# Kernel optimization log

Measured on AMD Instinct MI355X. Metric: run time of the kernel, lower is better.

## Reference

```python
import jax, jax.numpy as jnp
import numpy as np

EMBED_DIM = 1024
NUM_HEADS = 16
HEAD_DIM = EMBED_DIM // NUM_HEADS
THRESHOLD = 0.001
B, S = 8, 1024


def setup_inputs() -> dict:
    key = jax.random.key(0)
    ks = jax.random.split(key, 7)
    sc = 1.0 / np.sqrt(EMBED_DIM)
    return {
        "x": jax.random.normal(ks[0], (B, S, EMBED_DIM), dtype=jnp.float32),
        "Wq": jax.random.normal(ks[1], (NUM_HEADS, EMBED_DIM, HEAD_DIM), dtype=jnp.float32) * sc,
        "bq": jax.random.normal(ks[2], (NUM_HEADS, HEAD_DIM), dtype=jnp.float32) * 0.01,
        "Wk": jax.random.normal(ks[3], (NUM_HEADS, EMBED_DIM, HEAD_DIM), dtype=jnp.float32) * sc,
        "bk": jax.random.normal(ks[4], (NUM_HEADS, HEAD_DIM), dtype=jnp.float32) * 0.01,
        "Wv": jax.random.normal(ks[5], (NUM_HEADS, EMBED_DIM, HEAD_DIM), dtype=jnp.float32) * sc,
        "bv": jax.random.normal(ks[6], (NUM_HEADS, HEAD_DIM), dtype=jnp.float32) * 0.01,
    }


def thresholded_softmax(scores, threshold):
    # softmax over last dim, zero entries below threshold, renormalize
    s = jax.nn.softmax(scores, axis=-1)
    s = jnp.where(s < threshold, 0.0, s)
    return s / (jnp.sum(s, axis=-1, keepdims=True) + 1e-12)


def reference(x, Wq, bq, Wk, bk, Wv, bv):
    # x: [B,S,D]; Wq/Wk/Wv: [H,D,e]; biases: [H,e]
    scale = jnp.asarray(EMBED_DIM ** 0.5, x.dtype)  # note: scales by sqrt(embed_dim), not head_dim
    Q = jnp.einsum("bsd,hde->hbse", x, Wq) + bq[:, None, None, :]
    K = jnp.einsum("bsd,hde->hbse", x, Wk) + bk[:, None, None, :]
    V = jnp.einsum("bsd,hde->hbse", x, Wv) + bv[:, None, None, :]
    scores = jnp.einsum("hbse,hbte->hbst", Q, K) / scale  # [H,B,S,S]
    att = thresholded_softmax(scores, THRESHOLD)
    latent = jnp.einsum("hbst,hbte->hbse", att, V)  # [H,B,S,e]
    # concat heads along last dim in head order -> [B,S,H*e]
    residual = jnp.transpose(latent, (1, 2, 0, 3)).reshape(x.shape[0], x.shape[1], -1)
    x_res = x + residual  # dropout p=0.0 -> identity
    return (x_res, att)
```

## Files before the change

### kernel.cpp

```cpp
#include <hip/hip_runtime.h>
#include <hip/hip_bf16.h>
#include <cstdint>
#include <cstddef>

#define B_ 8
#define S_ 1024
#define H_ 16
#define E_ 64
#define D_ 1024

typedef unsigned short u16;
typedef short s16x8 __attribute__((ext_vector_type(8)));
typedef float f32x4 __attribute__((ext_vector_type(4)));

__device__ __forceinline__ u16 f2b(float f) {
  union { float f; unsigned u; } v; v.f = f;
  unsigned u = v.u;
  return (u16)((u + 0x7FFFu + ((u >> 16) & 1u)) >> 16);
}

__device__ __forceinline__ void gload16(const void* g, void* lds) {
  __builtin_amdgcn_global_load_lds(
      (const __attribute__((address_space(1))) void*)g,
      (__attribute__((address_space(3))) void*)lds, 16, 0, 0);
}

#define BARL() do {                                          \
  asm volatile("s_waitcnt lgkmcnt(0)" ::: "memory");         \
  __builtin_amdgcn_sched_barrier(0);                         \
  __builtin_amdgcn_s_barrier();                              \
  __builtin_amdgcn_sched_barrier(0);                         \
  asm volatile("" ::: "memory");                             \
} while (0)

__global__ void k_prep(const float* __restrict__ x, u16* __restrict__ xb,
                       const float* __restrict__ Wq, const float* __restrict__ Wk,
                       const float* __restrict__ Wv, u16* __restrict__ wbt) {
  if (blockIdx.x < 4096) {
    size_t i = ((size_t)blockIdx.x * 256 + threadIdx.x) * 8;
    float4 a = *(const float4*)(x + i);
    float4 b = *(const float4*)(x + i + 4);
    uint4 o;
    o.x = f2b(a.x) | ((unsigned)f2b(a.y) << 16);
    o.y = f2b(a.z) | ((unsigned)f2b(a.w) << 16);
    o.z = f2b(b.x) | ((unsigned)f2b(b.y) << 16);
    o.w = f2b(b.z) | ((unsigned)f2b(b.w) << 16);
    *(uint4*)(xb + i) = o;
    return;
  }
  __shared__ u16 T[64][65];
  int bid = blockIdx.x - 4096;
  int d0 = (bid & 15) * 64;
  int mh = bid >> 4;
  int mat = mh >> 4, h = mh & 15;
  const float* W = (mat == 0) ? Wq : (mat == 1) ? Wk : Wv;
  int tid = threadIdx.x;
#pragma unroll
  for (int rep = 0; rep < 4; rep++) {
    int dl = rep * 16 + (tid >> 4);
    int e0 = (tid & 15) * 4;
    float4 v = *(const float4*)(W + (size_t)h * (D_ * E_) + (size_t)(d0 + dl) * E_ + e0);
    T[dl][e0] = f2b(v.x); T[dl][e0 + 1] = f2b(v.y);
    T[dl][e0 + 2] = f2b(v.z); T[dl][e0 + 3] = f2b(v.w);
  }
  __syncthreads();
#pragma unroll
  for (int rep = 0; rep < 4; rep++) {
    int el = rep * 16 + (tid >> 4);
    int dl0 = (tid & 15) * 4;
    ushort4 o;
    o.x = T[dl0][el]; o.y = T[dl0 + 1][el]; o.z = T[dl0 + 2][el]; o.w = T[dl0 + 3][el];
    int n = mat * 1024 + h * 64 + el;
    *(ushort4*)(wbt + (size_t)n * D_ + d0 + dl0) = o;
  }
}

__global__ __launch_bounds__(256) void k_qkv(
    const u16* __restrict__ xb, const u16* __restrict__ wbt,
    const float* __restrict__ bq, const float* __restrict__ bk, const float* __restrict__ bv,
    u16* __restrict__ Qb, u16* __restrict__ Kb, u16* __restrict__ Vb) {
  __shared__ u16 As[128 * 64];
  __shared__ u16 Bs[128 * 64];
  int tid = threadIdx.x, l = tid & 63, w = tid >> 6;
  int bid = blockIdx.x;
  int xcd = bid & 7, i = bid >> 3;
  int m0 = (xcd * 8 + i / 24) * 128;
  int n0 = (i % 24) * 128;
  int wm = w >> 1, wn = w & 1;
  int rl = l & 15, kg = l >> 4;
  f32x4 acc[4][4] = {};
  for (int k0 = 0; k0 < D_; k0 += 64) {
#pragma unroll
    for (int i2 = 0; i2 < 4; i2++) {
      int ci = w * 4 + i2;
      int r = ci * 8 + (l >> 3);
      int c = (l & 7) ^ (r & 7);
      gload16(xb  + (size_t)(m0 + r) * D_ + k0 + c * 8, (char*)As + ci * 1024);
      gload16(wbt + (size_t)(n0 + r) * D_ + k0 + c * 8, (char*)Bs + ci * 1024);
    }
    __syncthreads();
#pragma unroll
    for (int kk = 0; kk < 2; kk++) {
      s16x8 af[4], bfr[4];
      int chunk = kk * 4 + kg;
#pragma unroll
      for (int fm = 0; fm < 4; fm++) {
        int r = wm * 64 + fm * 16 + rl;
        af[fm] = *(const s16x8*)(As + r * 64 + ((chunk ^ (r & 7)) * 8));
      }
#pragma unroll
      for (int fn = 0; fn < 4; fn++) {
        int r = wn * 64 + fn * 16 + rl;
        bfr[fn] = *(const s16x8*)(Bs + r * 64 + ((chunk ^ (r & 7)) * 8));
      }
#pragma unroll
      for (int fm = 0; fm < 4; fm++)
#pragma unroll
        for (int fn = 0; fn < 4; fn++)
          acc[fm][fn] = __builtin_amdgcn_mfma_f32_16x16x32_bf16(af[fm], bfr[fn], acc[fm][fn], 0, 0, 0);
    }
    __syncthreads();
  }
#pragma unroll
  for (int fn = 0; fn < 4; fn++) {
    int n = n0 + wn * 64 + fn * 16 + rl;
    int mat = n >> 10, h = (n >> 6) & 15, e = n & 63;
    const float* bias = (mat == 0) ? bq : (mat == 1) ? bk : bv;
    float bval = bias[h * 64 + e];
    u16* dst = (mat == 0) ? Qb : (mat == 1) ? Kb : Vb;
#pragma unroll
    for (int fm = 0; fm < 4; fm++)
#pragma unroll
      for (int j = 0; j < 4; j++) {
        int m = m0 + wm * 64 + fm * 16 + kg * 4 + j;
        int bb = m >> 10, s = m & 1023;
        dst[(size_t)((h * B_ + bb) * S_ + s) * E_ + e] = f2b(acc[fm][fn][j] + bval);
      }
  }
}

__global__ void k_vt(const u16* __restrict__ Vb, u16* __restrict__ Vt) {
  __shared__ u16 T[64][65];
  int hb = blockIdx.y, s0 = blockIdx.x * 64, tid = threadIdx.x;
  const u16* src = Vb + (size_t)hb * (S_ * E_);
#pragma unroll
  for (int rep = 0; rep < 4; rep++) {
    int sl = rep * 16 + (tid >> 4);
    int e0 = (tid & 15) * 4;
    ushort4 v = *(const ushort4*)(src + (size_t)(s0 + sl) * E_ + e0);
    T[sl][e0] = v.x; T[sl][e0 + 1] = v.y; T[sl][e0 + 2] = v.z; T[sl][e0 + 3] = v.w;
  }
  __syncthreads();
  u16* dst = Vt + (size_t)hb * (S_ * E_);
#pragma unroll
  for (int rep = 0; rep < 4; rep++) {
    int el = rep * 16 + (tid >> 4);
    int sl0 = (tid & 15) * 4;
    ushort4 o;
    o.x = T[sl0][el]; o.y = T[sl0 + 1][el]; o.z = T[sl0 + 2][el]; o.w = T[sl0 + 3][el];
    *(ushort4*)(dst + (size_t)el * S_ + s0 + sl0) = o;
  }
}

__global__ __launch_bounds__(512, 2) void f_attn(
    const u16* __restrict__ Qb, const u16* __restrict__ Kb, const u16* __restrict__ Vt,
    const float* __restrict__ x, float* __restrict__ att, float* __restrict__ out) {
  __shared__ u16 Qlds[64 * 64];
  __shared__ u16 KV[1024 * 64];
  __shared__ u16 Ab[2][64 * 64];
  __shared__ float red[3][64][4];

  int p = blockIdx.x;
  int L = (p & 7) * 256 + (p >> 3);
  int hb = L >> 4, mblk = L & 15;
  int m0 = mblk * 64;
  int tid = threadIdx.x, l = tid & 63, w = tid >> 6;
  int rl = l & 15, kg = l >> 4;
  int rh = w >> 2, cq = w & 3;

  const u16* Qp = Qb + (size_t)hb * (S_ * E_) + (size_t)m0 * E_;
  const u16* Kp = Kb + (size_t)hb * (S_ * E_);
  const u16* Vp = Vt + (size_t)hb * (S_ * E_);

  {
    int r = w * 8 + (l >> 3), c = (l & 7) ^ (r & 7);
    gload16(Qp + (size_t)r * E_ + c * 8, (char*)Qlds + w * 1024);
  }
#pragma unroll
  for (int i = 0; i < 16; i++) {
    int ci = w * 16 + i;
    int r = ci * 8 + (l >> 3), c = (l & 7) ^ (r & 7);
    gload16(Kp + (size_t)r * E_ + c * 8, (char*)KV + ci * 1024);
  }
  __syncthreads();

  s16x8 af[2][2];
#pragma unroll
  for (int fm = 0; fm < 2; fm++)
#pragma unroll
    for (int kk = 0; kk < 2; kk++) {
      int r = rh * 32 + fm * 16 + rl, ch = kk * 4 + kg;
      af[fm][kk] = *(const s16x8*)((const char*)Qlds + r * 128 + ((ch ^ (r & 7)) * 16));
    }

  f32x4 acc[2][16];
#pragma unroll
  for (int fm = 0; fm < 2; fm++)
#pragma unroll
    for (int ct = 0; ct < 16; ct++)
#pragma unroll
      for (int j = 0; j < 4; j++) acc[fm][ct][j] = 0.f;

#pragma unroll
  for (int ct = 0; ct < 16; ct++) {
    s16x8 bf[2];
#pragma unroll
    for (int kk = 0; kk < 2; kk++) {
      int r = ct * 64 + cq * 16 + rl, ch = kk * 4 + kg;
      bf[kk] = *(const s16x8*)((const char*)KV + r * 128 + ((ch ^ (r & 7)) * 16));
    }
#pragma unroll
    for (int fm = 0; fm < 2; fm++)
#pragma unroll
      for (int kk = 0; kk < 2; kk++)
        acc[fm][ct] = __builtin_amdgcn_mfma_f32_16x16x32_bf16(af[fm][kk], bf[kk], acc[fm][ct], 0, 0, 0);
  }
  __syncthreads();

#pragma unroll
  for (int i = 0; i < 16; i++) {
    int ci = w * 16 + i;
    int e = ci >> 1, hf = ci & 1;
    int c = ((hf * 64 + l) & ~7) | ((l & 7) ^ (e & 7));
    gload16(Vp + (size_t)e * S_ + c * 8, (char*)KV + e * 2048 + hf * 1024);
  }

  float mx[2][4], Z[2][4], Z2[2][4];
#pragma unroll
  for (int fm = 0; fm < 2; fm++)
#pragma unroll
    for (int j = 0; j < 4; j++) {
      float m = acc[fm][0][j];
#pragma unroll
      for (int ct = 1; ct < 16; ct++) m = fmaxf(m, acc[fm][ct][j]);
#pragma unroll
      for (int off = 8; off >= 1; off >>= 1) m = fmaxf(m, __shfl_xor(m, off));
      mx[fm][j] = m;
    }
  if (rl == 0) {
#pragma unroll
    for (int fm = 0; fm < 2; fm++)
#pragma unroll
      for (int j = 0; j < 4; j++) red[0][rh * 32 + fm * 16 + kg * 4 + j][cq] = mx[fm][j];
  }
  BARL();
#pragma unroll
  for (int fm = 0; fm < 2; fm++)
#pragma unroll
    for (int j = 0; j < 4; j++) {
      f32x4 r4 = *(const f32x4*)&red[0][rh * 32 + fm * 16 + kg * 4 + j][0];
      mx[fm][j] = fmaxf(fmaxf(r4[0], r4[1]), fmaxf(r4[2], r4[3]));
    }
#pragma unroll
  for (int fm = 0; fm < 2; fm++)
#pragma unroll
    for (int j = 0; j < 4; j++) {
      float s = 0.f;
#pragma unroll
      for (int ct = 0; ct < 16; ct++) {
        float e = __expf((acc[fm][ct][j] - mx[fm][j]) * 0.03125f);
        acc[fm][ct][j] = e;
        s += e;
      }
#pragma unroll
      for (int off = 8; off >= 1; off >>= 1) s += __shfl_xor(s, off);
      Z[fm][j] = s;
    }
  if (rl == 0) {
#pragma unroll
    for (int fm = 0; fm < 2; fm++)
#pragma unroll
      for (int j = 0; j < 4; j++) red[1][rh * 32 + fm * 16 + kg * 4 + j][cq] = Z[fm][j];
  }
  BARL();
#pragma unroll
  for (int fm = 0; fm < 2; fm++)
#pragma unroll
    for (int j = 0; j < 4; j++) {
      f32x4 r4 = *(const f32x4*)&red[1][rh * 32 + fm * 16 + kg * 4 + j][0];
      Z[fm][j] = r4[0] + r4[1] + r4[2] + r4[3];
    }
#pragma unroll
  for (int fm = 0; fm < 2; fm++)
#pragma unroll
    for (int j = 0; j < 4; j++) {
      float thr = 0.001f * Z[fm][j];
      float s = 0.f;
#pragma unroll
      for (int ct = 0; ct < 16; ct++) {
        float e = acc[fm][ct][j];
        e = (e >= thr) ? e : 0.f;
        acc[fm][ct][j] = e;
        s += e;
      }
#pragma unroll
      for (int off = 8; off >= 1; off >>= 1) s += __shfl_xor(s, off);
      Z2[fm][j] = s;
    }
  if (rl == 0) {
#pragma unroll
    for (int fm = 0; fm < 2; fm++)
#pragma unroll
      for (int j = 0; j < 4; j++) red[2][rh * 32 + fm * 16 + kg * 4 + j][cq] = Z2[fm][j];
  }
  BARL();
#pragma unroll
  for (int fm = 0; fm < 2; fm++)
#pragma unroll
    for (int j = 0; j < 4; j++) {
      f32x4 r4 = *(const f32x4*)&red[2][rh * 32 + fm * 16 + kg * 4 + j][0];
      float z2 = r4[0] + r4[1] + r4[2] + r4[3];
      float inv = 1.f / (z2 + 1e-12f * Z[fm][j]);
#pragma unroll
      for (int ct = 0; ct < 16; ct++) acc[fm][ct][j] *= inv;
    }

  asm volatile("s_waitcnt vmcnt(0)" ::: "memory");
  __builtin_amdgcn_sched_barrier(0);

  float* attp = att + ((size_t)hb << 20) + ((size_t)m0 << 10);
#pragma unroll
  for (int fm = 0; fm < 2; fm++)
#pragma unroll
    for (int j = 0; j < 4; j++) {
      int m = rh * 32 + fm * 16 + kg * 4 + j;
#pragma unroll
      for (int ct = 0; ct < 16; ct++)
        attp[((size_t)m << 10) + ct * 64 + cq * 16 + rl] = acc[fm][ct][j];
    }

  int mh2 = w >> 1, nh2 = w & 1;
  f32x4 acc2[2];
#pragma unroll
  for (int fn = 0; fn < 2; fn++)
#pragma unroll
    for (int j = 0; j < 4; j++) acc2[fn][j] = 0.f;

#pragma unroll
  for (int ct = 0; ct < 16; ct++) {
#pragma unroll
    for (int fm = 0; fm < 2; fm++)
#pragma unroll
      for (int j = 0; j < 4; j++) {
        int m = rh * 32 + fm * 16 + kg * 4 + j;
        int tl = cq * 16 + rl;
        int chw = tl >> 3;
        *(u16*)((char*)Ab[ct & 1] + m * 128 + ((chw ^ (m & 7)) * 16) + (tl & 7) * 2)
            = f2b(acc[fm][ct][j]);
      }
    BARL();
    s16x8 a2[2], b2[2][2];
#pragma unroll
    for (int kk = 0; kk < 2; kk++) {
      int ch = kk * 4 + kg;
      int rA = mh2 * 16 + rl;
      a2[kk] = *(const s16x8*)((const char*)Ab[ct & 1] + rA * 128 + ((ch ^ (rA & 7)) * 16));
#pragma unroll
      for (int fn = 0; fn < 2; fn++) {
        int e = nh2 * 32 + fn * 16 + rl;
        b2[fn][kk] = *(const s16x8*)((const char*)KV + e * 2048 + ct * 128 + ((ch ^ (e & 7)) * 16));
      }
    }
#pragma unroll
    for (int fn = 0; fn < 2; fn++)
#pragma unroll
      for (int kk = 0; kk < 2; kk++)
        acc2[fn] = __builtin_amdgcn_mfma_f32_16x16x32_bf16(a2[kk], b2[fn][kk], acc2[fn], 0, 0, 0);
  }

  int h = hb >> 3, bb = hb & 7;
#pragma unroll
  for (int fn = 0; fn < 2; fn++)
#pragma unroll
    for (int j = 0; j < 4; j++) {
      int m = m0 + mh2 * 16 + kg * 4 + j;
      int e = h * 64 + nh2 * 32 + fn * 16 + rl;
      size_t idx = (((size_t)bb * S_ + m) << 10) + e;
      out[idx] = x[idx] + acc2[fn][j];
    }
}

extern "C" void kernel_launch(void* const* d_in, const int* in_sizes, int n_in,
                              void* d_out, int out_size, void* d_ws, size_t ws_size,
                              hipStream_t stream) {
  const float* x  = (const float*)d_in[0];
  const float* Wq = (const float*)d_in[1];
  const float* bq = (const float*)d_in[2];
  const float* Wk = (const float*)d_in[3];
  const float* bk = (const float*)d_in[4];
  const float* Wv = (const float*)d_in[5];
  const float* bv = (const float*)d_in[6];
  float* xres = (float*)d_out;
  float* att  = xres + (size_t)B_ * S_ * D_;

  char* ws = (char*)d_ws;
  u16* xb  = (u16*)(ws);
  u16* wbt = (u16*)(ws + 16777216);
  u16* Qb  = (u16*)(ws + 23068672);
  u16* Kb  = (u16*)(ws + 39845888);
  u16* Vb  = (u16*)(ws + 56623104);
  u16* Vt  = (u16*)(ws);

  k_prep  <<<dim3(4864),    dim3(256), 0, stream>>>(x, xb, Wq, Wk, Wv, wbt);
  k_qkv   <<<dim3(1536),    dim3(256), 0, stream>>>(xb, wbt, bq, bk, bv, Qb, Kb, Vb);
  k_vt    <<<dim3(16, 128), dim3(256), 0, stream>>>(Vb, Vt);
  f_attn  <<<dim3(2048),    dim3(512), 0, stream>>>(Qb, Kb, Vt, x, att, xres);
}
```

Before: 299.3 us.

## Fuse V transpose into QKV epilogue and software-pipeline PV staging

The QKV GEMM epilogue now writes V directly in transposed [h,b,e,s] layout with 4-element vector stores, which removes the separate k_vt transpose kernel and its extra read and write of V. In the attention kernel, the bf16 conversion of the next probability tile into the LDS double buffer now overlaps the MFMAs of the current tile, with s_setprio raised around the MFMAs. Vt is moved to its own workspace region instead of aliasing xb. The risks are more divergent epilogue code and a barrier still taken on every iteration.

```diff
diff --git a/kernel.cpp b/kernel.cpp
--- a/kernel.cpp
+++ b/kernel.cpp
@@ -78,7 +78,7 @@
 __global__ __launch_bounds__(256) void k_qkv(
     const u16* __restrict__ xb, const u16* __restrict__ wbt,
     const float* __restrict__ bq, const float* __restrict__ bk, const float* __restrict__ bv,
-    u16* __restrict__ Qb, u16* __restrict__ Kb, u16* __restrict__ Vb) {
+    u16* __restrict__ Qb, u16* __restrict__ Kb, u16* __restrict__ Vt) {
   __shared__ u16 As[128 * 64];
   __shared__ u16 Bs[128 * 64];
   int tid = threadIdx.x, l = tid & 63, w = tid >> 6;
@@ -127,38 +127,29 @@
     int mat = n >> 10, h = (n >> 6) & 15, e = n & 63;
     const float* bias = (mat == 0) ? bq : (mat == 1) ? bk : bv;
     float bval = bias[h * 64 + e];
-    u16* dst = (mat == 0) ? Qb : (mat == 1) ? Kb : Vb;
-#pragma unroll
-    for (int fm = 0; fm < 4; fm++)
-#pragma unroll
-      for (int j = 0; j < 4; j++) {
-        int m = m0 + wm * 64 + fm * 16 + kg * 4 + j;
-        int bb = m >> 10, s = m & 1023;
-        dst[(size_t)((h * B_ + bb) * S_ + s) * E_ + e] = f2b(acc[fm][fn][j] + bval);
-      }
-  }
-}
-
-__global__ void k_vt(const u16* __restrict__ Vb, u16* __restrict__ Vt) {
-  __shared__ u16 T[64][65];
-  int hb = blockIdx.y, s0 = blockIdx.x * 64, tid = threadIdx.x;
-  const u16* src = Vb + (size_t)hb * (S_ * E_);
-#pragma unroll
-  for (int rep = 0; rep < 4; rep++) {
-    int sl = rep * 16 + (tid >> 4);
-    int e0 = (tid & 15) * 4;
-    ushort4 v = *(const ushort4*)(src + (size_t)(s0 + sl) * E_ + e0);
-    T[sl][e0] = v.x; T[sl][e0 + 1] = v.y; T[sl][e0 + 2] = v.z; T[sl][e0 + 3] = v.w;
-  }
-  __syncthreads();
-  u16* dst = Vt + (size_t)hb * (S_ * E_);
-#pragma unroll
-  for (int rep = 0; rep < 4; rep++) {
-    int el = rep * 16 + (tid >> 4);
-    int sl0 = (tid & 15) * 4;
-    ushort4 o;
-    o.x = T[sl0][el]; o.y = T[sl0 + 1][el]; o.z = T[sl0 + 2][el]; o.w = T[sl0 + 3][el];
-    *(ushort4*)(dst + (size_t)el * S_ + s0 + sl0) = o;
+    if (mat == 2) {
+#pragma unroll
+      for (int fm = 0; fm < 4; fm++) {
+        int sq = m0 + wm * 64 + fm * 16 + kg * 4;
+        int bb = sq >> 10, s = sq & 1023;
+        ushort4 o;
+        o.x = f2b(acc[fm][fn][0] + bval);
+        o.y = f2b(acc[fm][fn][1] + bval);
+        o.z = f2b(acc[fm][fn][2] + bval);
+        o.w = f2b(acc[fm][fn][3] + bval);
+        *(ushort4*)(Vt + ((size_t)((h * B_ + bb) * E_ + e) << 10) + s) = o;
+      }
+    } else {
+      u16* dst = (mat == 0) ? Qb : Kb;
+#pragma unroll
+      for (int fm = 0; fm < 4; fm++)
+#pragma unroll
+        for (int j = 0; j < 4; j++) {
+          int m = m0 + wm * 64 + fm * 16 + kg * 4 + j;
+          int bb = m >> 10, s = m & 1023;
+          dst[(size_t)((h * B_ + bb) * S_ + s) * E_ + e] = f2b(acc[fm][fn][j] + bval);
+        }
+    }
   }
 }
 
@@ -347,18 +338,18 @@
     for (int j = 0; j < 4; j++) acc2[fn][j] = 0.f;
 
 #pragma unroll
+  for (int fm = 0; fm < 2; fm++)
+#pragma unroll
+    for (int j = 0; j < 4; j++) {
+      int m = rh * 32 + fm * 16 + kg * 4 + j;
+      int tl = cq * 16 + rl;
+      *(u16*)((char*)Ab[0] + m * 128 + (((tl >> 3) ^ (m & 7)) * 16) + (tl & 7) * 2)
+          = f2b(acc[fm][0][j]);
+    }
+  BARL();
+
+#pragma unroll
   for (int ct = 0; ct < 16; ct++) {
-#pragma unroll
-    for (int fm = 0; fm < 2; fm++)
-#pragma unroll
-      for (int j = 0; j < 4; j++) {
-        int m = rh * 32 + fm * 16 + kg * 4 + j;
-        int tl = cq * 16 + rl;
-        int chw = tl >> 3;
-        *(u16*)((char*)Ab[ct & 1] + m * 128 + ((chw ^ (m & 7)) * 16) + (tl & 7) * 2)
-            = f2b(acc[fm][ct][j]);
-      }
-    BARL();
     s16x8 a2[2], b2[2][2];
 #pragma unroll
     for (int kk = 0; kk < 2; kk++) {
@@ -371,11 +362,25 @@
         b2[fn][kk] = *(const s16x8*)((const char*)KV + e * 2048 + ct * 128 + ((ch ^ (e & 7)) * 16));
       }
     }
+    if (ct < 15) {
+#pragma unroll
+      for (int fm = 0; fm < 2; fm++)
+#pragma unroll
+        for (int j = 0; j < 4; j++) {
+          int m = rh * 32 + fm * 16 + kg * 4 + j;
+          int tl = cq * 16 + rl;
+          *(u16*)((char*)Ab[(ct + 1) & 1] + m * 128 + (((tl >> 3) ^ (m & 7)) * 16) + (tl & 7) * 2)
+              = f2b(acc[fm][ct + 1][j]);
+        }
+    }
+    __builtin_amdgcn_s_setprio(1);
 #pragma unroll
     for (int fn = 0; fn < 2; fn++)
 #pragma unroll
       for (int kk = 0; kk < 2; kk++)
         acc2[fn] = __builtin_amdgcn_mfma_f32_16x16x32_bf16(a2[kk], b2[fn][kk], acc2[fn], 0, 0, 0);
+    __builtin_amdgcn_s_setprio(0);
+    BARL();
   }
 
   int h = hb >> 3, bb = hb & 7;
@@ -408,11 +413,9 @@
   u16* wbt = (u16*)(ws + 16777216);
   u16* Qb  = (u16*)(ws + 23068672);
   u16* Kb  = (u16*)(ws + 39845888);
-  u16* Vb  = (u16*)(ws + 56623104);
-  u16* Vt  = (u16*)(ws);
-
-  k_prep  <<<dim3(4864),    dim3(256), 0, stream>>>(x, xb, Wq, Wk, Wv, wbt);
-  k_qkv   <<<dim3(1536),    dim3(256), 0, stream>>>(xb, wbt, bq, bk, bv, Qb, Kb, Vb);
-  k_vt    <<<dim3(16, 128), dim3(256), 0, stream>>>(Vb, Vt);
-  f_attn  <<<dim3(2048),    dim3(512), 0, stream>>>(Qb, Kb, Vt, x, att, xres);
-}
+  u16* Vt  = (u16*)(ws + 56623104);
+
+  k_prep  <<<dim3(4864), dim3(256), 0, stream>>>(x, xb, Wq, Wk, Wv, wbt);
+  k_qkv   <<<dim3(1536), dim3(256), 0, stream>>>(xb, wbt, bq, bk, bv, Qb, Kb, Vt);
+  f_attn  <<<dim3(2048), dim3(512), 0, stream>>>(Qb, Kb, Vt, x, att, xres);
+}
```

After: 296.7 us. Within noise of the previous version (-0.9%).
